# Performance work log

Hardware: AMD Instinct MI355X
Metric: run time of the kernel (lower is better)

Reference implementation:

```python
import jax, jax.numpy as jnp
import numpy as np

B, S, T, K = 128, 4, 16, 36   # questions, answer slots (hardcoded 4), max tags/slot, num boxes
VD, QD, H = 256, 256, 256
NB = B * S * T                # total tag rows = leading dim of v, q


def setup_inputs() -> dict:
    key = jax.random.key(0)
    ks = jax.random.split(key, 8)
    tags_attention = jnp.ones((B, S, T), dtype=jnp.int32)  # all slots full -> sum == NB
    v = jax.random.normal(ks[0], (NB, K, VD), jnp.float32)
    q = jax.random.normal(ks[1], (NB, QD), jnp.float32)
    # binary box mask, first box always valid
    bm = (jax.random.uniform(ks[2], (B, K)) < 0.85).astype(jnp.float32)
    box_mask = bm.at[:, 0].set(1.0)
    Wv = jax.random.normal(ks[3], (H, VD), jnp.float32) / np.sqrt(VD).astype(np.float32)
    bv = jnp.zeros((H,), jnp.float32)
    Wq = jax.random.normal(ks[4], (H, QD), jnp.float32) / np.sqrt(QD).astype(np.float32)
    bq = jnp.zeros((H,), jnp.float32)
    Wl = jax.random.normal(ks[5], (1, H), jnp.float32) / np.sqrt(H).astype(np.float32)
    bl = jnp.zeros((1,), jnp.float32)
    return dict(v=v, q=q, box_mask=box_mask, tags_attention=tags_attention,
                Wv=Wv, bv=bv, Wq=Wq, bq=bq, Wl=Wl, bl=bl)


def reference(v, q, box_mask, tags_attention, Wv, bv, Wq, bq, Wl, bl):
    # FCNet projections (weight-normed Linear + ReLU; dropout inactive at eval)
    v_proj = jax.nn.relu(jnp.einsum('nkd,hd->nkh', v, Wv) + bv)          # [N,K,H]
    q_proj = jax.nn.relu(q @ Wq.T + bq)                                   # [N,H]
    joint = v_proj * q_proj[:, None, :]                                   # [N,K,H]
    logits = jnp.einsum('nkh,h->nk', joint, Wl[0]) + bl[0]                # [N,K]

    # pad_sequence: ragged rows -> [B,S,T,K] via per-slot offsets + masked gather
    Bq, Ss, Tt = tags_attention.shape
    lengths = tags_attention.sum(-1)                                      # [B,S]
    flat_len = lengths.reshape(-1)
    offsets = jnp.concatenate([jnp.zeros((1,), flat_len.dtype),
                               jnp.cumsum(flat_len)[:-1]]).reshape(Bq, Ss)
    t = jnp.arange(Tt)
    idx = offsets[:, :, None] + t                                         # [B,S,T]
    valid = t[None, None, :] < lengths[:, :, None]                        # [B,S,T]
    gathered = logits[jnp.clip(idx, 0, logits.shape[0] - 1)]              # [B,S,T,K]
    logits_batch = jnp.where(valid[..., None], gathered, 0.0)

    # masked_softmax (r2c style): softmax(x*mask)*mask, renormalized
    mask = box_mask[:, None, None, :]                                     # [B,1,1,K]
    w = jax.nn.softmax(logits_batch * mask, axis=-1) * mask
    w = w / (w.sum(-1, keepdims=True) + 1e-13)
    return w
```

## Files before the change

### kernel.cpp

```cpp
#include <hip/hip_runtime.h>
#include <hip/hip_bf16.h>
#include <stdint.h>

#define NBROWS 8192
#define KBOX   36
#define MROWS  (NBROWS * KBOX)
#define RPB    1152
#define NTILE  9

typedef __attribute__((ext_vector_type(8))) short bf16x8;
typedef __attribute__((ext_vector_type(4))) float f32x4;

__device__ __forceinline__ unsigned short f2bf(float f) {
  unsigned int u = __float_as_uint(f);
  return (unsigned short)((u + 0x7fffu + ((u >> 16) & 1u)) >> 16);
}

__device__ __forceinline__ unsigned int pk2(float x, float y) {
  __hip_bfloat16 hx = __float2bfloat16(x);
  __hip_bfloat16 hy = __float2bfloat16(y);
  unsigned short ux, uy;
  __builtin_memcpy(&ux, &hx, 2);
  __builtin_memcpy(&uy, &hy, 2);
  return (unsigned)ux | ((unsigned)uy << 16);
}

#define LGKM_BARRIER() do {                                   \
    asm volatile("s_waitcnt lgkmcnt(0)" ::: "memory");        \
    asm volatile("s_barrier" ::: "memory");                   \
  } while (0)

__global__ void cvt_kernel(const float* __restrict__ Wv, const float* __restrict__ Wq,
                           unsigned short* __restrict__ wvb, unsigned short* __restrict__ wqb) {
  int i = blockIdx.x * 256 + threadIdx.x;
  wvb[i] = f2bf(Wv[i]);
  wqb[i] = f2bf(Wq[i]);
}

__global__ __launch_bounds__(256, 2)
void qproj_kernel(const float* __restrict__ Amat,
                  const unsigned short* __restrict__ Wbf,
                  const float* __restrict__ bias,
                  const float* __restrict__ wl,
                  float* __restrict__ outp)
{
  __shared__ unsigned short Asm[2][64 * 32];
  __shared__ unsigned short Bsm[2][256 * 32];
  __shared__ float bias_sm[256];
  __shared__ float aux_sm[256];

  const int t    = threadIdx.x;
  const int lane = t & 63;
  const int wid  = t >> 6;
  const int r0   = blockIdx.x * 64;

  bias_sm[t] = bias[t];
  aux_sm[t]  = wl[t];

  const int brow = t >> 2;
  const int bko  = t & 3;
  const int arow = t >> 2;
  const int ako  = t & 3;
  const float* asrc = Amat + (size_t)(r0 + arow) * 256 + ako * 8;
  const int adst_off = arow * 32 + (ako ^ ((arow >> 1) & 3)) * 8;

  f32x4 acc[4][4];
  #pragma unroll
  for (int a = 0; a < 4; ++a)
    #pragma unroll
    for (int b = 0; b < 4; ++b) acc[a][b] = (f32x4)0.f;

  float4 aregA[2], aregB[2];
  uint4  breg[4];

  #pragma unroll
  for (int i = 0; i < 4; ++i)
    breg[i] = *(const uint4*)&Wbf[(brow + i * 64) * 256 + 0 + bko * 8];
  aregA[0] = ((const float4*)(asrc + 0))[0];
  aregA[1] = ((const float4*)(asrc + 0))[1];
  aregB[0] = ((const float4*)(asrc + 32))[0];
  aregB[1] = ((const float4*)(asrc + 32))[1];
  #pragma unroll
  for (int i = 0; i < 4; ++i) {
    int r = brow + i * 64;
    *(uint4*)&Bsm[0][r * 32 + (bko ^ ((r >> 1) & 3)) * 8] = breg[i];
  }
  {
    uint4 pk;
    pk.x = pk2(aregA[0].x, aregA[0].y);
    pk.y = pk2(aregA[0].z, aregA[0].w);
    pk.z = pk2(aregA[1].x, aregA[1].y);
    pk.w = pk2(aregA[1].z, aregA[1].w);
    *(uint4*)&Asm[0][adst_off] = pk;
  }
  LGKM_BARRIER();

  #pragma unroll
  for (int kk = 0; kk < 8; ++kk) {
    const int cur = kk & 1;
    if (kk < 7) {
      const int d0 = (kk + 1) * 32;
      #pragma unroll
      for (int i = 0; i < 4; ++i)
        breg[i] = *(const uint4*)&Wbf[(brow + i * 64) * 256 + d0 + bko * 8];
    }
    if (kk < 6) {
      const int d0 = (kk + 2) * 32;
      float4 t0 = ((const float4*)(asrc + d0))[0];
      float4 t1 = ((const float4*)(asrc + d0))[1];
      if (kk & 1) { aregB[0] = t0; aregB[1] = t1; }
      else        { aregA[0] = t0; aregA[1] = t1; }
    }
    bf16x8 af[4], bfr[4];
    #pragma unroll
    for (int mf = 0; mf < 4; ++mf) {
      int row  = mf * 16 + (lane & 15);
      int phys = (lane >> 4) ^ ((row >> 1) & 3);
      af[mf] = *(const bf16x8*)&Asm[cur][row * 32 + phys * 8];
    }
    #pragma unroll
    for (int nf = 0; nf < 4; ++nf) {
      int col  = wid * 64 + nf * 16 + (lane & 15);
      int phys = (lane >> 4) ^ ((col >> 1) & 3);
      bfr[nf] = *(const bf16x8*)&Bsm[cur][col * 32 + phys * 8];
    }
    #pragma unroll
    for (int mf = 0; mf < 4; ++mf)
      #pragma unroll
      for (int nf = 0; nf < 4; ++nf)
        acc[mf][nf] = __builtin_amdgcn_mfma_f32_16x16x32_bf16(af[mf], bfr[nf], acc[mf][nf], 0, 0, 0);
    if (kk < 7) {
      #pragma unroll
      for (int i = 0; i < 4; ++i) {
        int r = brow + i * 64;
        *(uint4*)&Bsm[1 - cur][r * 32 + (bko ^ ((r >> 1) & 3)) * 8] = breg[i];
      }
      const float4 a0 = (kk & 1) ? aregA[0] : aregB[0];
      const float4 a1 = (kk & 1) ? aregA[1] : aregB[1];
      uint4 pk;
      pk.x = pk2(a0.x, a0.y);
      pk.y = pk2(a0.z, a0.w);
      pk.z = pk2(a1.x, a1.y);
      pk.w = pk2(a1.z, a1.w);
      *(uint4*)&Asm[1 - cur][adst_off] = pk;
      LGKM_BARRIER();
    }
  }

  #pragma unroll
  for (int mf = 0; mf < 4; ++mf)
    #pragma unroll
    for (int nf = 0; nf < 4; ++nf) {
      int col = wid * 64 + nf * 16 + (lane & 15);
      float bb = bias_sm[col];
      float ww = aux_sm[col];
      #pragma unroll
      for (int j = 0; j < 4; ++j) {
        int row = mf * 16 + ((lane >> 4) << 2) + j;
        float x = fmaxf(acc[mf][nf][j] + bb, 0.f) * ww;
        outp[(size_t)(r0 + row) * 256 + col] = x;
      }
    }
}

__global__ __launch_bounds__(512, 2)
void vmain_kernel(const float* __restrict__ v,
                  const unsigned short* __restrict__ Wbf,
                  const float* __restrict__ bv,
                  const float* __restrict__ g,
                  const float* __restrict__ blp,
                  const float* __restrict__ bmask,
                  float* __restrict__ outp)
{
  __shared__ unsigned short Wlds[256 * 256];
  __shared__ unsigned short Asm[2][128 * 32];
  __shared__ float gtile[5 * 256];
  __shared__ float partial[128 * 4];
  __shared__ float logit_sm[RPB];

  const int t    = threadIdx.x;
  const int lane = t & 63;
  const int wid  = t >> 6;
  const int wn   = wid & 3;
  const int wm   = wid >> 2;
  const int l15  = lane & 15;
  const int lq   = lane >> 4;
  const int blk  = blockIdx.x;
  const long long rowbase = (long long)blk * RPB;

  #pragma unroll
  for (int p = 0; p < 16; ++p) {
    int flat = p * 512 + t;
    int col  = flat >> 5;
    int chk  = flat & 31;
    uint4 w = *(const uint4*)&Wbf[col * 256 + chk * 8];
    *(uint4*)&Wlds[col * 256 + (chk ^ (col & 7)) * 8] = w;
  }

  float bias_r[4];
  #pragma unroll
  for (int nf = 0; nf < 4; ++nf) bias_r[nf] = bv[wn * 64 + nf * 16 + l15];
  const float blv = blp[0];

  const int arow = t >> 2;
  const int ako  = t & 3;
  const float* asrc = v + (rowbase + arow) * 256 + ako * 8;
  const int adst = arow * 32 + (ako ^ ((arow >> 1) & 3)) * 8;

  float4 pA0[2], pA1[2];

  pA0[0] = ((const float4*)(asrc + 0))[0];
  pA0[1] = ((const float4*)(asrc + 0))[1];
  pA1[0] = ((const float4*)(asrc + 32))[0];
  pA1[1] = ((const float4*)(asrc + 32))[1];
  {
    uint4 pk;
    pk.x = pk2(pA0[0].x, pA0[0].y);
    pk.y = pk2(pA0[0].z, pA0[0].w);
    pk.z = pk2(pA0[1].x, pA0[1].y);
    pk.w = pk2(pA0[1].z, pA0[1].w);
    *(uint4*)&Asm[0][adst] = pk;
  }
  LGKM_BARRIER();

  f32x4 acc[4][4];
  float gr[3];

  #pragma unroll 1
  for (int tile = 0; tile < NTILE; ++tile) {
    #pragma unroll
    for (int a = 0; a < 4; ++a)
      #pragma unroll
      for (int b = 0; b < 4; ++b) acc[a][b] = (f32x4)0.f;

    const int m0  = (int)rowbase + tile * 128;
    const int n0t = m0 / KBOX;

    #pragma unroll
    for (int kk = 0; kk < 8; ++kk) {
      const int cur = kk & 1;
      {
        const float* p = nullptr;
        if (kk < 6)                  p = asrc + tile * 32768 + (kk + 2) * 32;
        else if (tile < NTILE - 1)   p = asrc + (tile + 1) * 32768 + (kk - 6) * 32;
        if (p) {
          float4 t0 = ((const float4*)p)[0];
          float4 t1 = ((const float4*)p)[1];
          if (kk & 1) { pA1[0] = t0; pA1[1] = t1; }
          else        { pA0[0] = t0; pA0[1] = t1; }
        }
      }
      if (kk == 0) {
        #pragma unroll
        for (int i = 0; i < 3; ++i) {
          int idx = i * 512 + t;
          if (idx < 1280) {
            int n = n0t + (idx >> 8);
            if (n > NBROWS - 1) n = NBROWS - 1;
            gr[i] = g[(size_t)n * 256 + (idx & 255)];
          }
        }
      }
      bf16x8 af[4], bfr[4];
      #pragma unroll
      for (int mf = 0; mf < 4; ++mf) {
        int row  = wm * 64 + mf * 16 + l15;
        int phys = lq ^ ((row >> 1) & 3);
        af[mf] = *(const bf16x8*)&Asm[cur][row * 32 + phys * 8];
      }
      #pragma unroll
      for (int nf = 0; nf < 4; ++nf) {
        int col  = wn * 64 + nf * 16 + l15;
        int phys = (kk * 4 + lq) ^ (col & 7);
        bfr[nf] = *(const bf16x8*)&Wlds[col * 256 + phys * 8];
      }
      #pragma unroll
      for (int mf = 0; mf < 4; ++mf)
        #pragma unroll
        for (int nf = 0; nf < 4; ++nf)
          acc[mf][nf] = __builtin_amdgcn_mfma_f32_16x16x32_bf16(af[mf], bfr[nf], acc[mf][nf], 0, 0, 0);
      if (kk < 7 || tile < NTILE - 1) {
        const float4 a0 = (kk & 1) ? pA0[0] : pA1[0];
        const float4 a1 = (kk & 1) ? pA0[1] : pA1[1];
        uint4 pk;
        pk.x = pk2(a0.x, a0.y);
        pk.y = pk2(a0.z, a0.w);
        pk.z = pk2(a1.x, a1.y);
        pk.w = pk2(a1.z, a1.w);
        *(uint4*)&Asm[1 - cur][adst] = pk;
      }
      if (kk == 1) {
        #pragma unroll
        for (int i = 0; i < 3; ++i) {
          int idx = i * 512 + t;
          if (idx < 1280) gtile[idx] = gr[i];
        }
      }
      if (kk == 7) {
        #pragma unroll
        for (int mf = 0; mf < 4; ++mf)
          #pragma unroll
          for (int j = 0; j < 4; ++j) {
            int rloc = wm * 64 + mf * 16 + lq * 4 + j;
            int nloc = (m0 + rloc) / KBOX - n0t;
            const float* grow = &gtile[nloc * 256];
            float sv = 0.f;
            #pragma unroll
            for (int nf = 0; nf < 4; ++nf) {
              int col = wn * 64 + nf * 16 + l15;
              sv += fmaxf(acc[mf][nf][j] + bias_r[nf], 0.f) * grow[col];
            }
            sv += __shfl_xor(sv, 1);
            sv += __shfl_xor(sv, 2);
            sv += __shfl_xor(sv, 4);
            sv += __shfl_xor(sv, 8);
            if (l15 == 0) partial[rloc * 4 + wn] = sv;
          }
      }
      LGKM_BARRIER();
      if (kk == 7 && t < 128) {
        logit_sm[tile * 128 + t] = partial[t * 4 + 0] + partial[t * 4 + 1]
                                 + partial[t * 4 + 2] + partial[t * 4 + 3] + blv;
      }
    }
  }

  LGKM_BARRIER();

  const int batch = blk >> 1;
  #pragma unroll
  for (int i = 0; i < 4; ++i) {
    int bx = wid * 4 + i;
    long long bg = (long long)blk * 32 + bx;
    float mk = 0.f, lv = 0.f;
    if (lane < KBOX) {
      mk = bmask[batch * KBOX + lane];
      lv = logit_sm[bx * KBOX + lane];
    }
    bool act = (lane < KBOX) && (mk > 0.5f);
    float lm = act ? lv : -3.0e38f;
    #pragma unroll
    for (int off = 32; off >= 1; off >>= 1) lm = fmaxf(lm, __shfl_xor(lm, off));
    float e = act ? expf(lv - lm) : 0.f;
    float ssum = e;
    #pragma unroll
    for (int off = 32; off >= 1; off >>= 1) ssum += __shfl_xor(ssum, off);
    if (lane < KBOX) outp[bg * KBOX + lane] = e / ssum;
  }
}

extern "C" void kernel_launch(void* const* d_in, const int* in_sizes, int n_in,
                              void* d_out, int out_size, void* d_ws, size_t ws_size,
                              hipStream_t stream) {
  const float* v        = (const float*)d_in[0];
  const float* q        = (const float*)d_in[1];
  const float* box_mask = (const float*)d_in[2];
  const float* Wv = (const float*)d_in[4];
  const float* bv = (const float*)d_in[5];
  const float* Wq = (const float*)d_in[6];
  const float* bq = (const float*)d_in[7];
  const float* Wl = (const float*)d_in[8];
  const float* bl = (const float*)d_in[9];
  float* outp = (float*)d_out;

  char* ws = (char*)d_ws;
  unsigned short* wvb = (unsigned short*)ws;
  unsigned short* wqb = (unsigned short*)(ws + 131072);
  float* g = (float*)(ws + 262144);

  cvt_kernel<<<256, 256, 0, stream>>>(Wv, Wq, wvb, wqb);
  qproj_kernel<<<NBROWS / 64, 256, 0, stream>>>(q, wqb, bq, Wl, g);
  vmain_kernel<<<256, 512, 0, stream>>>(v, wvb, bv, g, bl, box_mask, outp);
}
```

Baseline: 114.4 us.

## Load A fragments directly from global into registers, drop LDS staging and barriers

Each wave now reads its own MFMA A-operand fragments straight from global memory into registers, converts them to bf16 in-register, and double-buffers them across k-steps. This removes the shared-memory A tile, the per-k-step block barriers and the gtile staging, which now go to global directly in the epilogue. There is one barrier per tile, using a double-buffered partial array. The cost is that each wave in the 4 column groups (wn) now loads the same A rows again, quadrupling global/L2 traffic for v. It also uses more registers for the prefetch buffers.

After: 220.8 us. +93.0%, slower.

```diff
diff --git a/kernel.cpp b/kernel.cpp
--- a/kernel.cpp
+++ b/kernel.cpp
@@ -173,9 +173,7 @@
                   float* __restrict__ outp)
 {
   __shared__ unsigned short Wlds[256 * 256];
-  __shared__ unsigned short Asm[2][128 * 32];
-  __shared__ float gtile[5 * 256];
-  __shared__ float partial[128 * 4];
+  __shared__ float partial[2][128 * 4];
   __shared__ float logit_sm[RPB];
 
   const int t    = threadIdx.x;
@@ -202,29 +200,46 @@
   for (int nf = 0; nf < 4; ++nf) bias_r[nf] = bv[wn * 64 + nf * 16 + l15];
   const float blv = blp[0];
 
-  const int arow = t >> 2;
-  const int ako  = t & 3;
-  const float* asrc = v + (rowbase + arow) * 256 + ako * 8;
-  const int adst = arow * 32 + (ako ^ ((arow >> 1) & 3)) * 8;
-
-  float4 pA0[2], pA1[2];
-
-  pA0[0] = ((const float4*)(asrc + 0))[0];
-  pA0[1] = ((const float4*)(asrc + 0))[1];
-  pA1[0] = ((const float4*)(asrc + 32))[0];
-  pA1[1] = ((const float4*)(asrc + 32))[1];
-  {
-    uint4 pk;
-    pk.x = pk2(pA0[0].x, pA0[0].y);
-    pk.y = pk2(pA0[0].z, pA0[0].w);
-    pk.z = pk2(pA0[1].x, pA0[1].y);
-    pk.w = pk2(pA0[1].z, pA0[1].w);
-    *(uint4*)&Asm[0][adst] = pk;
-  }
+  const float* arow0 = v + (rowbase + wm * 64 + l15) * 256 + lq * 8;
+
+  f32x4 acc[4][4];
+  float4 pfA[4][2], pfB[4][2];
+
+  auto issueFrag = [&](int nt, int nk, float4 (&pf)[4][2]) {
+    const float* base = arow0 + nt * 32768 + nk * 32;
+    #pragma unroll
+    for (int mf = 0; mf < 4; ++mf) {
+      const float* p = base + mf * 4096;
+      pf[mf][0] = ((const float4*)p)[0];
+      pf[mf][1] = ((const float4*)p)[1];
+    }
+  };
+
+  auto mfmaStep = [&](int kk, float4 (&pf)[4][2]) {
+    bf16x8 bfr[4];
+    #pragma unroll
+    for (int nf = 0; nf < 4; ++nf) {
+      int col  = wn * 64 + nf * 16 + l15;
+      int phys = (kk * 4 + lq) ^ (col & 7);
+      bfr[nf] = *(const bf16x8*)&Wlds[col * 256 + phys * 8];
+    }
+    #pragma unroll
+    for (int mf = 0; mf < 4; ++mf) {
+      uint4 pk;
+      pk.x = pk2(pf[mf][0].x, pf[mf][0].y);
+      pk.y = pk2(pf[mf][0].z, pf[mf][0].w);
+      pk.z = pk2(pf[mf][1].x, pf[mf][1].y);
+      pk.w = pk2(pf[mf][1].z, pf[mf][1].w);
+      bf16x8 af;
+      __builtin_memcpy(&af, &pk, 16);
+      #pragma unroll
+      for (int nf = 0; nf < 4; ++nf)
+        acc[mf][nf] = __builtin_amdgcn_mfma_f32_16x16x32_bf16(af, bfr[nf], acc[mf][nf], 0, 0, 0);
+    }
+  };
+
   LGKM_BARRIER();
-
-  f32x4 acc[4][4];
-  float gr[3];
+  issueFrag(0, 0, pfA);
 
   #pragma unroll 1
   for (int tile = 0; tile < NTILE; ++tile) {
@@ -233,95 +248,41 @@
       #pragma unroll
       for (int b = 0; b < 4; ++b) acc[a][b] = (f32x4)0.f;
 
+    const bool more = (tile + 1) < NTILE;
+    issueFrag(tile, 1, pfB);  mfmaStep(0, pfA);
+    issueFrag(tile, 2, pfA);  mfmaStep(1, pfB);
+    issueFrag(tile, 3, pfB);  mfmaStep(2, pfA);
+    issueFrag(tile, 4, pfA);  mfmaStep(3, pfB);
+    issueFrag(tile, 5, pfB);  mfmaStep(4, pfA);
+    issueFrag(tile, 6, pfA);  mfmaStep(5, pfB);
+    issueFrag(tile, 7, pfB);  mfmaStep(6, pfA);
+    if (more) issueFrag(tile + 1, 0, pfA);
+    mfmaStep(7, pfB);
+
     const int m0  = (int)rowbase + tile * 128;
-    const int n0t = m0 / KBOX;
-
-    #pragma unroll
-    for (int kk = 0; kk < 8; ++kk) {
-      const int cur = kk & 1;
-      {
-        const float* p = nullptr;
-        if (kk < 6)                  p = asrc + tile * 32768 + (kk + 2) * 32;
-        else if (tile < NTILE - 1)   p = asrc + (tile + 1) * 32768 + (kk - 6) * 32;
-        if (p) {
-          float4 t0 = ((const float4*)p)[0];
-          float4 t1 = ((const float4*)p)[1];
-          if (kk & 1) { pA1[0] = t0; pA1[1] = t1; }
-          else        { pA0[0] = t0; pA0[1] = t1; }
+    const int p   = tile & 1;
+    #pragma unroll
+    for (int mf = 0; mf < 4; ++mf)
+      #pragma unroll
+      for (int j = 0; j < 4; ++j) {
+        int rloc = wm * 64 + mf * 16 + lq * 4 + j;
+        int n    = (m0 + rloc) / KBOX;
+        float sv = 0.f;
+        #pragma unroll
+        for (int nf = 0; nf < 4; ++nf) {
+          int col = wn * 64 + nf * 16 + l15;
+          sv += fmaxf(acc[mf][nf][j] + bias_r[nf], 0.f) * g[(size_t)n * 256 + col];
         }
+        sv += __shfl_xor(sv, 1);
+        sv += __shfl_xor(sv, 2);
+        sv += __shfl_xor(sv, 4);
+        sv += __shfl_xor(sv, 8);
+        if (l15 == 0) partial[p][rloc * 4 + wn] = sv;
       }
-      if (kk == 0) {
-        #pragma unroll
-        for (int i = 0; i < 3; ++i) {
-          int idx = i * 512 + t;
-          if (idx < 1280) {
-            int n = n0t + (idx >> 8);
-            if (n > NBROWS - 1) n = NBROWS - 1;
-            gr[i] = g[(size_t)n * 256 + (idx & 255)];
-          }
-        }
-      }
-      bf16x8 af[4], bfr[4];
-      #pragma unroll
-      for (int mf = 0; mf < 4; ++mf) {
-        int row  = wm * 64 + mf * 16 + l15;
-        int phys = lq ^ ((row >> 1) & 3);
-        af[mf] = *(const bf16x8*)&Asm[cur][row * 32 + phys * 8];
-      }
-      #pragma unroll
-      for (int nf = 0; nf < 4; ++nf) {
-        int col  = wn * 64 + nf * 16 + l15;
-        int phys = (kk * 4 + lq) ^ (col & 7);
-        bfr[nf] = *(const bf16x8*)&Wlds[col * 256 + phys * 8];
-      }
-      #pragma unroll
-      for (int mf = 0; mf < 4; ++mf)
-        #pragma unroll
-        for (int nf = 0; nf < 4; ++nf)
-          acc[mf][nf] = __builtin_amdgcn_mfma_f32_16x16x32_bf16(af[mf], bfr[nf], acc[mf][nf], 0, 0, 0);
-      if (kk < 7 || tile < NTILE - 1) {
-        const float4 a0 = (kk & 1) ? pA0[0] : pA1[0];
-        const float4 a1 = (kk & 1) ? pA0[1] : pA1[1];
-        uint4 pk;
-        pk.x = pk2(a0.x, a0.y);
-        pk.y = pk2(a0.z, a0.w);
-        pk.z = pk2(a1.x, a1.y);
-        pk.w = pk2(a1.z, a1.w);
-        *(uint4*)&Asm[1 - cur][adst] = pk;
-      }
-      if (kk == 1) {
-        #pragma unroll
-        for (int i = 0; i < 3; ++i) {
-          int idx = i * 512 + t;
-          if (idx < 1280) gtile[idx] = gr[i];
-        }
-      }
-      if (kk == 7) {
-        #pragma unroll
-        for (int mf = 0; mf < 4; ++mf)
-          #pragma unroll
-          for (int j = 0; j < 4; ++j) {
-            int rloc = wm * 64 + mf * 16 + lq * 4 + j;
-            int nloc = (m0 + rloc) / KBOX - n0t;
-            const float* grow = &gtile[nloc * 256];
-            float sv = 0.f;
-            #pragma unroll
-            for (int nf = 0; nf < 4; ++nf) {
-              int col = wn * 64 + nf * 16 + l15;
-              sv += fmaxf(acc[mf][nf][j] + bias_r[nf], 0.f) * grow[col];
-            }
-            sv += __shfl_xor(sv, 1);
-            sv += __shfl_xor(sv, 2);
-            sv += __shfl_xor(sv, 4);
-            sv += __shfl_xor(sv, 8);
-            if (l15 == 0) partial[rloc * 4 + wn] = sv;
-          }
-      }
-      LGKM_BARRIER();
-      if (kk == 7 && t < 128) {
-        logit_sm[tile * 128 + t] = partial[t * 4 + 0] + partial[t * 4 + 1]
-                                 + partial[t * 4 + 2] + partial[t * 4 + 3] + blv;
-      }
+    LGKM_BARRIER();
+    if (t < 128) {
+      logit_sm[tile * 128 + t] = partial[p][t * 4 + 0] + partial[p][t * 4 + 1]
+                               + partial[p][t * 4 + 2] + partial[p][t * 4 + 3] + blv;
     }
   }
 
```
